# Optimization experiments

Hardware: AMD Instinct MI355X
Metric: run time of the kernel (lower is better)

Reference implementation:

```python
import jax, jax.numpy as jnp
import numpy as np

V, E, H = 50257, 256, 512
B, S = 4, 512


def setup_inputs() -> dict:
    key = jax.random.key(0)
    ks = jax.random.split(key, 16)
    k_ih = 1.0 / np.sqrt(H)
    inp = {
        "input_ids": jax.random.randint(ks[0], (B, S), 0, V, dtype=jnp.int64) if jax.config.jax_enable_x64 else jax.random.randint(ks[0], (B, S), 0, V, dtype=jnp.int32),
        "embedding": jax.random.normal(ks[1], (V, E), jnp.float32) * 0.02,
        "W_ih": jax.random.uniform(ks[2], (3 * H, E), jnp.float32, -k_ih, k_ih),
        "W_hh": jax.random.uniform(ks[3], (3 * H, H), jnp.float32, -k_ih, k_ih),
        "b_ih": jax.random.uniform(ks[4], (3 * H,), jnp.float32, -k_ih, k_ih),
        "b_hh": jax.random.uniform(ks[5], (3 * H,), jnp.float32, -k_ih, k_ih),
        "W_he": jax.random.normal(ks[6], (E, H), jnp.float32) * 0.02,
        "b_he": jnp.zeros((E,), jnp.float32),
        "output_bias": jnp.zeros((V,), jnp.float32),
        "W_read": jax.random.normal(ks[7], (1, H), jnp.float32) * 0.02,
        "b_read": jnp.zeros((1,), jnp.float32),
        "W_write": jax.random.normal(ks[8], (1, H), jnp.float32) * 0.02,
        "b_write": jnp.zeros((1,), jnp.float32),
        "W_decay": jax.random.normal(ks[9], (1, H), jnp.float32) * 0.02,
        "b_decay": jnp.zeros((1,), jnp.float32),
        "memory_scale": jnp.asarray(4.0, jnp.float32),
    }
    return inp


def _gru(x, W_ih, W_hh, b_ih, b_hh):
    # x: [B,S,E] -> states [B,S,H], PyTorch GRU gate order (r, z, n)
    xg = jnp.einsum("bse,ge->bsg", x, W_ih) + b_ih  # [B,S,3H]

    def step(h, xg_t):
        hg = h @ W_hh.T + b_hh
        xr, xz, xn = jnp.split(xg_t, 3, axis=-1)
        hr, hz, hn = jnp.split(hg, 3, axis=-1)
        r = jax.nn.sigmoid(xr + hr)
        z = jax.nn.sigmoid(xz + hz)
        n = jnp.tanh(xn + r * hn)
        h_new = (1.0 - z) * n + z * h
        return h_new, h_new

    h0 = jnp.zeros((x.shape[0], W_hh.shape[1]), x.dtype)
    _, states = jax.lax.scan(step, h0, jnp.swapaxes(xg, 0, 1))
    return jnp.swapaxes(states, 0, 1)  # [B,S,H]


def reference(input_ids, embedding, W_ih, W_hh, b_ih, b_hh, W_he, b_he,
              output_bias, W_read, b_read, W_write, b_write, W_decay, b_decay,
              memory_scale):
    emb = embedding[input_ids]                      # [B,S,E]
    states = _gru(emb, W_ih, W_hh, b_ih, b_hh)      # [B,S,H]
    proj = jnp.einsum("bsh,eh->bse", states, W_he) + b_he
    base = jnp.einsum("bse,ve->bsv", proj, embedding) + output_bias  # [B,S,V]

    read = jax.nn.sigmoid(jnp.einsum("bsh,oh->bso", states, W_read) + b_read) * memory_scale
    decay = jax.nn.sigmoid(jnp.einsum("bsh,oh->bso", states, W_decay) + b_decay)
    write = jax.nn.sigmoid(jnp.einsum("bsh,oh->bso", states, W_write) + b_write)

    bsz = base.shape[0]
    rows = jnp.arange(bsz)

    def step(m, xs):
        base_t, read_t, decay_t, write_t, ids_t = xs
        out = base_t + read_t * m                   # read before write
        m = m * decay_t
        m = m.at[rows, ids_t].add(write_t[:, 0])
        return m, out

    xs = (jnp.swapaxes(base, 0, 1), jnp.swapaxes(read, 0, 1),
          jnp.swapaxes(decay, 0, 1), jnp.swapaxes(write, 0, 1),
          jnp.swapaxes(input_ids, 0, 1))
    m0 = jnp.zeros((bsz, base.shape[2]), base.dtype)
    _, outs = jax.lax.scan(step, m0, xs)            # [S,B,V]
    return jnp.swapaxes(outs, 0, 1)                 # [B,S,V]
```

## Files before the change

### kernel.cpp

```cpp
#include <hip/hip_runtime.h>
#include <hip/hip_bf16.h>
#include <hip/hip_fp16.h>
#include <math.h>

#define V_SIZE 50257
#define V_PAD  50304
#define E_DIM  256
#define H_DIM  512
#define G_DIM  1536
#define B_SZ   4
#define S_LEN  512

typedef __attribute__((ext_vector_type(8))) short bf16x8;
typedef __attribute__((ext_vector_type(4))) float f32x4;
typedef __attribute__((ext_vector_type(2))) _Float16 h16x2;

__device__ __forceinline__ float sigmoidf_(float x) { return 1.0f / (1.0f + expf(-x)); }
__device__ __forceinline__ float fsig(float x) { return 1.0f / (1.0f + __expf(-x)); }
__device__ __forceinline__ float ftanh(float x) { return 1.0f - 2.0f / (__expf(2.0f * x) + 1.0f); }

__device__ __forceinline__ h16x2 as_h2(unsigned int u) {
  union { unsigned int u; h16x2 h; } x; x.u = u; return x.h;
}
#if defined(__has_builtin)
#if __has_builtin(__builtin_amdgcn_fdot2)
#define HAVE_FDOT2 1
#endif
#endif
__device__ __forceinline__ float fdot2_(unsigned int a, unsigned int b, float c) {
#ifdef HAVE_FDOT2
  return __builtin_amdgcn_fdot2(as_h2(a), as_h2(b), c, false);
#else
  h16x2 ha = as_h2(a), hb = as_h2(b);
  return c + (float)ha[0] * (float)hb[0] + (float)ha[1] * (float)hb[1];
#endif
}
__device__ __forceinline__ void gload_lds16(const void* g, void* l) {
  __builtin_amdgcn_global_load_lds((const __attribute__((address_space(1))) unsigned int*)g,
                                   (__attribute__((address_space(3))) unsigned int*)l, 16, 0, 0);
}

__global__ __launch_bounds__(256) void k_xg(const int* __restrict__ ids, const float* __restrict__ emb,
                                            const float* __restrict__ W_ih, const float* __restrict__ b_ih,
                                            float* __restrict__ xg) {
  __shared__ float embs[16][260];
  __shared__ float wl[64][133];
  const int g0 = blockIdx.x * 128, n0 = blockIdx.y * 16, tid = threadIdx.x;
  for (int idx = tid; idx < 16 * 256; idx += 256) {
    int n = idx >> 8, e = idx & 255;
    embs[n][e] = emb[(long)ids[n0 + n] * E_DIM + e];
  }
  const int g = tid & 127, ng = tid >> 7;
  float acc[8] = {0.f,0.f,0.f,0.f,0.f,0.f,0.f,0.f};
  for (int e0 = 0; e0 < 256; e0 += 64) {
    __syncthreads();
    for (int idx = tid; idx < 128 * 64; idx += 256) {
      int r = idx >> 6, c = idx & 63;
      wl[c][r] = W_ih[(long)(g0 + r) * E_DIM + e0 + c];
    }
    __syncthreads();
    for (int c = 0; c < 64; ++c) {
      float w = wl[c][g];
      #pragma unroll
      for (int j = 0; j < 8; ++j) acc[j] += w * embs[ng * 8 + j][e0 + c];
    }
  }
  const float bias = b_ih[g0 + g];
  #pragma unroll
  for (int j = 0; j < 8; ++j) {
    int n = n0 + ng * 8 + j;
    xg[(long)n * G_DIM + g0 + g] = acc[j] + bias;
  }
}

#define NWG 32
#define NEXTRA 216
#define WROWU 261
#define WPLU  (16 * WROWU)
#define HROWU 260
__global__ __launch_bounds__(512, 1) void k_scan(const float* __restrict__ xg,
                                                 const float* __restrict__ W_hh,
                                                 const float* __restrict__ b_hh,
                                                 float* __restrict__ states,
                                                 unsigned long long* __restrict__ h_hist,
                                                 const float* __restrict__ emb,
                                                 __hip_bfloat16* __restrict__ emb_bf) {
  __shared__ unsigned int Wp[3 * WPLU];
  __shared__ unsigned int hp[4 * HROWU];
  __shared__ float red[2][8][16][12];
  const int bid = blockIdx.x, tid = threadIdx.x;

  if (bid >= NWG) {
    const long total = (long)V_PAD * E_DIM;
    for (long i = (long)(bid - NWG) * 512 + tid; i < total; i += (long)NEXTRA * 512) {
      int row = (int)(i >> 8);
      float v = (row < V_SIZE) ? emb[i] : 0.0f;
      emb_bf[i] = __float2bfloat16(v);
    }
    return;
  }

  const int wg = bid;
  const int i0 = wg * 16;
  for (int e = tid; e < 3 * 16 * 256; e += 512) {
    int q = e >> 12, i = (e >> 8) & 15, p = e & 255;
    float2 w2 = reinterpret_cast<const float2*>(W_hh + (long)((q << 9) + i0 + i) * H_DIM)[p];
    unsigned int pk = (unsigned int)__half_as_ushort(__float2half(w2.x)) |
                      ((unsigned int)__half_as_ushort(__float2half(w2.y)) << 16);
    Wp[q * WPLU + i * WROWU + p] = pk;
  }
  const int wave = tid >> 6, l = tid & 63, il = l >> 2, part = l & 3;
  const int ii = tid >> 2, bb = tid & 3;
  const int pidx = tid >> 1;
  float h_prev = 0.0f;
  float bhr = 0.f, bhz = 0.f, bhn = 0.f;
  if (tid < 64) { bhr = b_hh[i0 + ii]; bhz = b_hh[512 + i0 + ii]; bhn = b_hh[1024 + i0 + ii]; }
  __syncthreads();

  for (int t = 0; t < S_LEN; ++t) {
    float xr_v = 0.f, xz_v = 0.f, xn_v = 0.f;
    if (tid < 64) {
      const float* xgrow = xg + (long)(bb * S_LEN + t) * G_DIM + i0 + ii;
      xr_v = xgrow[0]; xz_v = xgrow[512]; xn_v = xgrow[1024];
    }
    float acc[3][4] = {{0.f,0.f,0.f,0.f},{0.f,0.f,0.f,0.f},{0.f,0.f,0.f,0.f}};
    if (t > 0) {
      const unsigned long long* hb = h_hist + (long)(t - 1) * 512;
      unsigned long long v;
      do {
        v = __hip_atomic_load(hb + tid, __ATOMIC_RELAXED, __HIP_MEMORY_SCOPE_AGENT);
      } while (v == 0xFFFFFFFFFFFFFFFFull);
      const unsigned int lo = (unsigned int)v, hi = (unsigned int)(v >> 32);
      const unsigned int plo = __shfl_xor(lo, 1), phi = __shfl_xor(hi, 1);
      if ((tid & 1) == 0) {
        hp[pidx]         = (lo & 0xffffu) | (plo << 16);
        hp[HROWU + pidx] = (lo >> 16) | (plo & 0xffff0000u);
      } else {
        hp[2 * HROWU + pidx] = (phi & 0xffffu) | (hi << 16);
        hp[3 * HROWU + pidx] = (phi >> 16) | (hi & 0xffff0000u);
      }
      const int pbase = (wave << 5) + (part << 3);
      #pragma unroll
      for (int j = 0; j < 8; ++j) {
        const int p = pbase + j;
        const unsigned int w_r = Wp[il * WROWU + p];
        const unsigned int w_z = Wp[WPLU + il * WROWU + p];
        const unsigned int w_n = Wp[2 * WPLU + il * WROWU + p];
        const unsigned int h0 = hp[p];
        const unsigned int h1 = hp[HROWU + p];
        const unsigned int h2 = hp[2 * HROWU + p];
        const unsigned int h3 = hp[3 * HROWU + p];
        acc[0][0] = fdot2_(w_r, h0, acc[0][0]); acc[0][1] = fdot2_(w_r, h1, acc[0][1]);
        acc[0][2] = fdot2_(w_r, h2, acc[0][2]); acc[0][3] = fdot2_(w_r, h3, acc[0][3]);
        acc[1][0] = fdot2_(w_z, h0, acc[1][0]); acc[1][1] = fdot2_(w_z, h1, acc[1][1]);
        acc[1][2] = fdot2_(w_z, h2, acc[1][2]); acc[1][3] = fdot2_(w_z, h3, acc[1][3]);
        acc[2][0] = fdot2_(w_n, h0, acc[2][0]); acc[2][1] = fdot2_(w_n, h1, acc[2][1]);
        acc[2][2] = fdot2_(w_n, h2, acc[2][2]); acc[2][3] = fdot2_(w_n, h3, acc[2][3]);
      }
    }
    #pragma unroll
    for (int q = 0; q < 3; ++q)
      #pragma unroll
      for (int b = 0; b < 4; ++b) {
        float v = acc[q][b];
        v += __shfl_xor(v, 1);
        v += __shfl_xor(v, 2);
        if (part == 0) red[t & 1][wave][il][q * 4 + b] = v;
      }
    __syncthreads();
    if (tid < 64) {
      float hr = bhr, hz = bhz, hn = bhn;
      #pragma unroll
      for (int w = 0; w < 8; ++w) {
        hr += red[t & 1][w][ii][0 + bb];
        hz += red[t & 1][w][ii][4 + bb];
        hn += red[t & 1][w][ii][8 + bb];
      }
      float r  = fsig(xr_v + hr);
      float z  = fsig(xz_v + hz);
      float nn = ftanh(xn_v + r * hn);
      float h_new = (1.0f - z) * nn + z * h_prev;
      h_prev = h_new;
      unsigned int hu = (unsigned int)__half_as_ushort(__float2half(h_new));
      unsigned int v1 = __shfl_down(hu, 1);
      unsigned int v2 = __shfl_down(hu, 2);
      unsigned int v3 = __shfl_down(hu, 3);
      if (bb == 0) {
        unsigned long long pk = (unsigned long long)(hu | (v1 << 16)) |
                                ((unsigned long long)(v2 | (v3 << 16)) << 32);
        __hip_atomic_store(h_hist + (long)t * 512 + i0 + ii, pk,
                           __ATOMIC_RELAXED, __HIP_MEMORY_SCOPE_AGENT);
      }
      states[(long)(bb * S_LEN + t) * H_DIM + i0 + ii] = h_new;
    }
  }
}

__global__ __launch_bounds__(256) void k_projgates(const float* __restrict__ states,
     const float* __restrict__ W_he, const float* __restrict__ b_he,
     __hip_bfloat16* __restrict__ proj,
     const float* __restrict__ W_read, const float* __restrict__ b_read,
     const float* __restrict__ W_write, const float* __restrict__ b_write,
     const float* __restrict__ W_decay, const float* __restrict__ b_decay,
     const float* __restrict__ mscale,
     float* __restrict__ read_s, float* __restrict__ decay_s, float* __restrict__ write_s) {
  __shared__ float sm[6464];
  const int bid = blockIdx.x, tid = threadIdx.x;
  if (bid < 256) {
    float* sts = sm;
    float* wle = sm + 2048;
    const int n0 = (bid & 63) * 32, e0 = (bid >> 6) * 64;
    const int e = tid & 63, ng = tid >> 6;
    float acc[8] = {0.f,0.f,0.f,0.f,0.f,0.f,0.f,0.f};
    for (int h0 = 0; h0 < 512; h0 += 64) {
      __syncthreads();
      for (int idx = tid; idx < 32 * 64; idx += 256) {
        int n = idx >> 6, c = idx & 63;
        sts[n * 64 + c] = states[(long)(n0 + n) * H_DIM + h0 + c];
      }
      for (int idx = tid; idx < 64 * 64; idx += 256) {
        int r = idx >> 6, c = idx & 63;
        wle[c * 69 + r] = W_he[(long)(e0 + r) * H_DIM + h0 + c];
      }
      __syncthreads();
      for (int c = 0; c < 64; ++c) {
        float w = wle[c * 69 + e];
        #pragma unroll
        for (int j = 0; j < 8; ++j) acc[j] += w * sts[(ng * 8 + j) * 64 + c];
      }
    }
    const float bias = b_he[e0 + e];
    #pragma unroll
    for (int j = 0; j < 8; ++j) {
      int n = n0 + ng * 8 + j;
      proj[(long)n * E_DIM + e0 + e] = __float2bfloat16(acc[j] + bias);
    }
  } else {
    float* wr = sm; float* ww = sm + 512; float* wd = sm + 1024;
    for (int i = tid; i < 512; i += 256) { wr[i] = W_read[i]; ww[i] = W_write[i]; wd[i] = W_decay[i]; }
    __syncthreads();
    const int wave = tid >> 6, l = tid & 63;
    const float br = b_read[0], bw = b_write[0], bd = b_decay[0], ms = mscale[0];
    for (int r = 0; r < 16; ++r) {
      const int n = (bid - 256) * 64 + wave * 16 + r;
      const float* st = states + (long)n * H_DIM;
      float ar = 0.f, aw = 0.f, ad = 0.f;
      #pragma unroll
      for (int h0 = 0; h0 < 512; h0 += 64) {
        float s = st[h0 + l];
        ar += s * wr[h0 + l]; aw += s * ww[h0 + l]; ad += s * wd[h0 + l];
      }
      #pragma unroll
      for (int k = 1; k < 64; k <<= 1) {
        ar += __shfl_xor(ar, k); aw += __shfl_xor(aw, k); ad += __shfl_xor(ad, k);
      }
      if (l == 0) {
        read_s[n]  = sigmoidf_(ar + br) * ms;
        write_s[n] = sigmoidf_(aw + bw);
        decay_s[n] = sigmoidf_(ad + bd);
      }
    }
  }
}

__global__ __launch_bounds__(256) void k_base(const __hip_bfloat16* __restrict__ A,
                                              const __hip_bfloat16* __restrict__ Bm,
                                              const float* __restrict__ obias,
                                              float* __restrict__ C) {
  __shared__ unsigned short As[128 * 32], Bs[128 * 32];
  const int swz = (blockIdx.x & 7) * 786 + (blockIdx.x >> 3);
  const int m0 = (swz & 15) * 128, n0 = (swz >> 4) * 128;
  const int tid = threadIdx.x;
  const int wid = tid >> 6, l = tid & 63;
  const int wm = wid >> 1, wn = wid & 1;
  f32x4 acc[4][4];
  #pragma unroll
  for (int mi = 0; mi < 4; ++mi)
    #pragma unroll
    for (int ni = 0; ni < 4; ++ni) acc[mi][ni] = (f32x4){0.f, 0.f, 0.f, 0.f};

  for (int kk = 0; kk < 256; kk += 32) {
    __syncthreads();
    #pragma unroll
    for (int s = 0; s < 2; ++s) {
      const int cibase = wid * 128 + s * 64;
      const int ci = cibase + l;
      const int row = ci >> 2, cq = ci & 3;
      gload_lds16(A + (long)(m0 + row) * E_DIM + kk + cq * 8, As + cibase * 8);
      gload_lds16(Bm + (long)(n0 + row) * E_DIM + kk + cq * 8, Bs + cibase * 8);
    }
    __syncthreads();
    bf16x8 af[4], bfr[4];
    const int krow = (l >> 4) * 8;
    #pragma unroll
    for (int mi = 0; mi < 4; ++mi) {
      int row = wm * 64 + mi * 16 + (l & 15);
      af[mi] = *reinterpret_cast<const bf16x8*>(&As[row * 32 + krow]);
    }
    #pragma unroll
    for (int ni = 0; ni < 4; ++ni) {
      int row = wn * 64 + ni * 16 + (l & 15);
      bfr[ni] = *reinterpret_cast<const bf16x8*>(&Bs[row * 32 + krow]);
    }
    #pragma unroll
    for (int mi = 0; mi < 4; ++mi)
      #pragma unroll
      for (int ni = 0; ni < 4; ++ni)
        acc[mi][ni] = __builtin_amdgcn_mfma_f32_16x16x32_bf16(af[mi], bfr[ni], acc[mi][ni], 0, 0, 0);
  }
  #pragma unroll
  for (int mi = 0; mi < 4; ++mi) {
    const int rowb = m0 + wm * 64 + mi * 16 + (l >> 4) * 4;
    #pragma unroll
    for (int ni = 0; ni < 4; ++ni) {
      const int col = n0 + wn * 64 + ni * 16 + (l & 15);
      if (col < V_SIZE) {
        const float ob = obias[col];
        #pragma unroll
        for (int r = 0; r < 4; ++r)
          C[(long)(rowb + r) * V_SIZE + col] = acc[mi][ni][r] + ob;
      }
    }
  }
}

__global__ __launch_bounds__(64) void k_corr(const int* __restrict__ ids,
                                             const float* __restrict__ read_s,
                                             const float* __restrict__ decay_s,
                                             const float* __restrict__ write_s,
                                             float* __restrict__ out) {
  __shared__ int ids_s[512];
  __shared__ float rd[512], dc[512], wrs[512], c[512];
  const int b = blockIdx.x, j = blockIdx.y, l = threadIdx.x;
  for (int t = l; t < 512; t += 64) {
    int n = b * 512 + t;
    ids_s[t] = ids[n]; rd[t] = read_s[n]; dc[t] = decay_s[n]; wrs[t] = write_s[n];
  }
  __syncthreads();
  const int v = ids_s[j];
  bool own = true;
  for (int jj = l; jj < j; jj += 64) if (ids_s[jj] == v) own = false;
  if (!__all(own)) return;
  if (l == 0) {
    float m = wrs[j];
    for (int t = j + 1; t < 512; ++t) {
      c[t] = rd[t] * m;
      m *= dc[t];
      if (ids_s[t] == v) m += wrs[t];
    }
  }
  __syncthreads();
  float* outb = out + (long)b * S_LEN * V_SIZE + v;
  for (int t = j + 1 + l; t < 512; t += 64)
    outb[(long)t * V_SIZE] += c[t];
}

extern "C" void kernel_launch(void* const* d_in, const int* in_sizes, int n_in,
                              void* d_out, int out_size, void* d_ws, size_t ws_size,
                              hipStream_t stream) {
  const int*   ids     = (const int*)d_in[0];
  const float* emb     = (const float*)d_in[1];
  const float* W_ih    = (const float*)d_in[2];
  const float* W_hh    = (const float*)d_in[3];
  const float* b_ih    = (const float*)d_in[4];
  const float* b_hh    = (const float*)d_in[5];
  const float* W_he    = (const float*)d_in[6];
  const float* b_he    = (const float*)d_in[7];
  const float* obias   = (const float*)d_in[8];
  const float* W_read  = (const float*)d_in[9];
  const float* b_read  = (const float*)d_in[10];
  const float* W_write = (const float*)d_in[11];
  const float* b_write = (const float*)d_in[12];
  const float* W_decay = (const float*)d_in[13];
  const float* b_decay = (const float*)d_in[14];
  const float* mscale  = (const float*)d_in[15];

  char* ws = (char*)d_ws;
  __hip_bfloat16* emb_bf  = (__hip_bfloat16*)ws;
  __hip_bfloat16* proj_bf = (__hip_bfloat16*)(ws + 25755648);
  float* read_s  = (float*)(ws + 26804224);
  float* decay_s = (float*)(ws + 26812416);
  float* write_s = (float*)(ws + 26820608);

  char* ob = (char*)d_out;
  float* xg     = (float*)ob;
  float* states = (float*)(ob + 12582912);
  unsigned long long* h_hist = (unsigned long long*)(ob + 16777216);
  float* out = (float*)d_out;

  hipMemsetAsync(h_hist, 0xFF, (size_t)S_LEN * 512 * sizeof(unsigned long long), stream);
  dim3 gxg(12, 128);
  k_xg<<<gxg, 256, 0, stream>>>(ids, emb, W_ih, b_ih, xg);
  k_scan<<<NWG + NEXTRA, 512, 0, stream>>>(xg, W_hh, b_hh, states, h_hist, emb, emb_bf);
  k_projgates<<<288, 256, 0, stream>>>(states, W_he, b_he, proj_bf,
                                       W_read, b_read, W_write, b_write, W_decay, b_decay,
                                       mscale, read_s, decay_s, write_s);
  k_base<<<6288, 256, 0, stream>>>(proj_bf, emb_bf, obias, out);
  dim3 gc(4, 512);
  k_corr<<<gc, 64, 0, stream>>>(ids, read_s, decay_s, write_s, out);
}
```

Measured before the change: 1.645 ms.

## Fuse input-gate GEMM into scan kernel with flag-polled producer/consumer overlap

Removes the separate k_xg launch and computes the input-gate projection inside extra workgroups of the scan kernel. Those workgroups write xg with agent-scope atomic stores, ordered by timestep, while the recurrent workgroups spin on a 0xFF sentinel until their xg row is ready. This overlaps the GEMM with the sequential scan. It also changes the h_hist poll into a pipelined sequence of four outstanding atomic loads to cut polling latency. The costs are an extra memset of xg, fewer workgroups left for the bf16 embedding conversion, and correctness that relies on the xg workgroups running alongside the scan workgroups.

```diff
diff --git a/kernel.cpp b/kernel.cpp
--- a/kernel.cpp
+++ b/kernel.cpp
@@ -39,60 +39,35 @@
   __builtin_amdgcn_global_load_lds((const __attribute__((address_space(1))) unsigned int*)g,
                                    (__attribute__((address_space(3))) unsigned int*)l, 16, 0, 0);
 }
-
-__global__ __launch_bounds__(256) void k_xg(const int* __restrict__ ids, const float* __restrict__ emb,
-                                            const float* __restrict__ W_ih, const float* __restrict__ b_ih,
-                                            float* __restrict__ xg) {
-  __shared__ float embs[16][260];
-  __shared__ float wl[64][133];
-  const int g0 = blockIdx.x * 128, n0 = blockIdx.y * 16, tid = threadIdx.x;
-  for (int idx = tid; idx < 16 * 256; idx += 256) {
-    int n = idx >> 8, e = idx & 255;
-    embs[n][e] = emb[(long)ids[n0 + n] * E_DIM + e];
-  }
-  const int g = tid & 127, ng = tid >> 7;
-  float acc[8] = {0.f,0.f,0.f,0.f,0.f,0.f,0.f,0.f};
-  for (int e0 = 0; e0 < 256; e0 += 64) {
-    __syncthreads();
-    for (int idx = tid; idx < 128 * 64; idx += 256) {
-      int r = idx >> 6, c = idx & 63;
-      wl[c][r] = W_ih[(long)(g0 + r) * E_DIM + e0 + c];
-    }
-    __syncthreads();
-    for (int c = 0; c < 64; ++c) {
-      float w = wl[c][g];
-      #pragma unroll
-      for (int j = 0; j < 8; ++j) acc[j] += w * embs[ng * 8 + j][e0 + c];
-    }
-  }
-  const float bias = b_ih[g0 + g];
-  #pragma unroll
-  for (int j = 0; j < 8; ++j) {
-    int n = n0 + ng * 8 + j;
-    xg[(long)n * G_DIM + g0 + g] = acc[j] + bias;
-  }
+__device__ __forceinline__ unsigned int ld_agent(const unsigned int* p) {
+  return __hip_atomic_load(p, __ATOMIC_RELAXED, __HIP_MEMORY_SCOPE_AGENT);
+}
+__device__ __forceinline__ void st_agent(unsigned int* p, unsigned int v) {
+  __hip_atomic_store(p, v, __ATOMIC_RELAXED, __HIP_MEMORY_SCOPE_AGENT);
 }
 
 #define NWG 32
-#define NEXTRA 216
+#define NXGB 96
 #define WROWU 261
 #define WPLU  (16 * WROWU)
 #define HROWU 260
-__global__ __launch_bounds__(512, 1) void k_scan(const float* __restrict__ xg,
+#define RED(buf,w,i,k) red_[((((buf)*8+(w))*16+(i))*12)+(k)]
+__global__ __launch_bounds__(512, 1) void k_scan(const int* __restrict__ ids,
+                                                 const float* __restrict__ emb,
+                                                 const float* __restrict__ W_ih,
+                                                 const float* __restrict__ b_ih,
+                                                 float* __restrict__ xg,
                                                  const float* __restrict__ W_hh,
                                                  const float* __restrict__ b_hh,
                                                  float* __restrict__ states,
                                                  unsigned long long* __restrict__ h_hist,
-                                                 const float* __restrict__ emb,
                                                  __hip_bfloat16* __restrict__ emb_bf) {
-  __shared__ unsigned int Wp[3 * WPLU];
-  __shared__ unsigned int hp[4 * HROWU];
-  __shared__ float red[2][8][16][12];
+  __shared__ char smraw[66560];
   const int bid = blockIdx.x, tid = threadIdx.x;
 
-  if (bid >= NWG) {
+  if (bid >= NWG + NXGB) {
     const long total = (long)V_PAD * E_DIM;
-    for (long i = (long)(bid - NWG) * 512 + tid; i < total; i += (long)NEXTRA * 512) {
+    for (long i = (long)(bid - NWG - NXGB) * 512 + tid; i < total; i += (long)128 * 512) {
       int row = (int)(i >> 8);
       float v = (row < V_SIZE) ? emb[i] : 0.0f;
       emb_bf[i] = __float2bfloat16(v);
@@ -100,6 +75,48 @@
     return;
   }
 
+  if (bid >= NWG) {
+    float* embs_ = (float*)smraw;
+    float* wl_   = (float*)(smraw + 16640);
+    unsigned int* xg_u = (unsigned int*)xg;
+    const int g = tid & 127, ng = tid >> 7;
+    for (int tau = bid - NWG; tau < 1536; tau += NXGB) {
+      const int cidx = tau / 12, gidx = tau % 12;
+      const int b = cidx & 3, sc = cidx >> 2;
+      const int n0 = b * 512 + sc * 16, g0 = gidx * 128;
+      __syncthreads();
+      for (int idx = tid; idx < 16 * 256; idx += 512) {
+        int n = idx >> 8, e = idx & 255;
+        embs_[n * 260 + e] = emb[(long)ids[n0 + n] * E_DIM + e];
+      }
+      float acc[4] = {0.f, 0.f, 0.f, 0.f};
+      for (int e0 = 0; e0 < 256; e0 += 64) {
+        __syncthreads();
+        for (int idx = tid; idx < 128 * 64; idx += 512) {
+          int r = idx >> 6, c = idx & 63;
+          wl_[c * 133 + r] = W_ih[(long)(g0 + r) * E_DIM + e0 + c];
+        }
+        __syncthreads();
+        for (int c = 0; c < 64; ++c) {
+          float w = wl_[c * 133 + g];
+          #pragma unroll
+          for (int j = 0; j < 4; ++j) acc[j] += w * embs_[(ng * 4 + j) * 260 + e0 + c];
+        }
+      }
+      const float bias = b_ih[g0 + g];
+      #pragma unroll
+      for (int j = 0; j < 4; ++j) {
+        int n = n0 + ng * 4 + j;
+        union { float f; unsigned int u; } pv; pv.f = acc[j] + bias;
+        st_agent(xg_u + (long)n * G_DIM + g0 + g, pv.u);
+      }
+    }
+    return;
+  }
+
+  unsigned int* Wp = (unsigned int*)smraw;
+  unsigned int* hp = (unsigned int*)(smraw + 50112);
+  float* red_ = (float*)(smraw + 54272);
   const int wg = bid;
   const int i0 = wg * 16;
   for (int e = tid; e < 3 * 16 * 256; e += 512) {
@@ -120,16 +137,30 @@
   for (int t = 0; t < S_LEN; ++t) {
     float xr_v = 0.f, xz_v = 0.f, xn_v = 0.f;
     if (tid < 64) {
-      const float* xgrow = xg + (long)(bb * S_LEN + t) * G_DIM + i0 + ii;
-      xr_v = xgrow[0]; xz_v = xgrow[512]; xn_v = xgrow[1024];
+      const unsigned int* xgu = (const unsigned int*)xg + ((long)(bb * S_LEN + t) * G_DIM + i0 + ii);
+      unsigned int a0, a1, a2;
+      do {
+        a0 = ld_agent(xgu);
+        a1 = ld_agent(xgu + 512);
+        a2 = ld_agent(xgu + 1024);
+      } while (a0 == 0xFFFFFFFFu || a1 == 0xFFFFFFFFu || a2 == 0xFFFFFFFFu);
+      union { unsigned int u; float f; } c0, c1, c2;
+      c0.u = a0; c1.u = a1; c2.u = a2;
+      xr_v = c0.f; xz_v = c1.f; xn_v = c2.f;
     }
     float acc[3][4] = {{0.f,0.f,0.f,0.f},{0.f,0.f,0.f,0.f},{0.f,0.f,0.f,0.f}};
     if (t > 0) {
-      const unsigned long long* hb = h_hist + (long)(t - 1) * 512;
+      const unsigned long long* hb = h_hist + (long)(t - 1) * 512 + tid;
+      unsigned long long s0 = __hip_atomic_load(hb, __ATOMIC_RELAXED, __HIP_MEMORY_SCOPE_AGENT);
+      unsigned long long s1 = __hip_atomic_load(hb, __ATOMIC_RELAXED, __HIP_MEMORY_SCOPE_AGENT);
+      unsigned long long s2 = __hip_atomic_load(hb, __ATOMIC_RELAXED, __HIP_MEMORY_SCOPE_AGENT);
+      unsigned long long s3 = __hip_atomic_load(hb, __ATOMIC_RELAXED, __HIP_MEMORY_SCOPE_AGENT);
       unsigned long long v;
-      do {
-        v = __hip_atomic_load(hb + tid, __ATOMIC_RELAXED, __HIP_MEMORY_SCOPE_AGENT);
-      } while (v == 0xFFFFFFFFFFFFFFFFull);
+      while (true) {
+        if (s0 != 0xFFFFFFFFFFFFFFFFull) { v = s0; break; }
+        s0 = s1; s1 = s2; s2 = s3;
+        s3 = __hip_atomic_load(hb, __ATOMIC_RELAXED, __HIP_MEMORY_SCOPE_AGENT);
+      }
       const unsigned int lo = (unsigned int)v, hi = (unsigned int)(v >> 32);
       const unsigned int plo = __shfl_xor(lo, 1), phi = __shfl_xor(hi, 1);
       if ((tid & 1) == 0) {
@@ -165,16 +196,16 @@
         float v = acc[q][b];
         v += __shfl_xor(v, 1);
         v += __shfl_xor(v, 2);
-        if (part == 0) red[t & 1][wave][il][q * 4 + b] = v;
+        if (part == 0) RED(t & 1, wave, il, q * 4 + b) = v;
       }
     __syncthreads();
     if (tid < 64) {
       float hr = bhr, hz = bhz, hn = bhn;
       #pragma unroll
       for (int w = 0; w < 8; ++w) {
-        hr += red[t & 1][w][ii][0 + bb];
-        hz += red[t & 1][w][ii][4 + bb];
-        hn += red[t & 1][w][ii][8 + bb];
+        hr += RED(t & 1, w, ii, 0 + bb);
+        hz += RED(t & 1, w, ii, 4 + bb);
+        hn += RED(t & 1, w, ii, 8 + bb);
       }
       float r  = fsig(xr_v + hr);
       float z  = fsig(xz_v + hz);
@@ -389,9 +420,8 @@
   float* out = (float*)d_out;
 
   hipMemsetAsync(h_hist, 0xFF, (size_t)S_LEN * 512 * sizeof(unsigned long long), stream);
-  dim3 gxg(12, 128);
-  k_xg<<<gxg, 256, 0, stream>>>(ids, emb, W_ih, b_ih, xg);
-  k_scan<<<NWG + NEXTRA, 512, 0, stream>>>(xg, W_hh, b_hh, states, h_hist, emb, emb_bf);
+  hipMemsetAsync(xg, 0xFF, (size_t)2048 * G_DIM * sizeof(float), stream);
+  k_scan<<<256, 512, 0, stream>>>(ids, emb, W_ih, b_ih, xg, W_hh, b_hh, states, h_hist, emb_bf);
   k_projgates<<<288, 256, 0, stream>>>(states, W_he, b_he, proj_bf,
                                        W_read, b_read, W_write, b_write, W_decay, b_decay,
                                        mscale, read_s, decay_s, write_s);
```

Result: slower. 2.453 ms (+49.1%).
